# Performance work log

Measured on AMD Instinct MI355X. Metric: run time of the kernel, lower is better.

## Reference

```python
import jax, jax.numpy as jnp
import numpy as np

B, H, S, D = 4, 16, 2048, 64

def setup_inputs() -> dict:
    key = jax.random.key(0)
    kq, kk, kv = jax.random.split(key, 3)
    return {
        "input_query": jax.random.normal(kq, (B, H, S, D), dtype=jnp.float32),
        "input_key": jax.random.normal(kk, (B, H, S, D), dtype=jnp.float32),
        "input_value": jax.random.normal(kv, (B, H, S, D), dtype=jnp.float32),
    }

def reference(input_query, input_key, input_value):
    # Unscaled, unmasked attention: softmax(Q K^T) V
    scores = jnp.einsum("bhsd,bhtd->bhst", input_query, input_key)  # [B,H,S,S]
    probs = jax.nn.softmax(scores, axis=-1)
    return jnp.einsum("bhst,bhtd->bhsd", probs, input_value)  # [B,H,S,D]
```

## Files before the change

kernel.cpp:

```cpp
#include <hip/hip_runtime.h>
#include <hip/hip_bf16.h>
#include <stdint.h>

#define SEQ 2048
#define DIM 64
#define NH  64
#define KT  32
#define NT  (SEQ / KT)
#define RAW_BYTES  16384
#define FRAG_BYTES 12288
#define KF_BYTES   8192

typedef __attribute__((ext_vector_type(8)))  short    bf16x8;
typedef __attribute__((ext_vector_type(8)))  _Float16 f16x8;
typedef __attribute__((ext_vector_type(16))) float    f32x16;
typedef unsigned int u32;

#if __has_builtin(__builtin_amdgcn_exp2f)
#define EXP2(x) __builtin_amdgcn_exp2f(x)
#else
#define EXP2(x) exp2f(x)
#endif

__device__ __forceinline__ int phi(int s) {
    int h = (s >> 2) & 1, b = s >> 3, i = s & 3;
    return 8 * h + 4 * b + i + (b >= 2 ? 8 : 0);
}
__device__ __forceinline__ short f2bf(float f) {
    union { float f; u32 u; } v; v.f = f;
    u32 r = v.u + 0x7fffu + ((v.u >> 16) & 1u);
    return (short)(r >> 16);
}

__device__ __forceinline__ void stage_tile(const float* gK, const float* gV,
                                           char* raw, int wave, int lane) {
    #pragma unroll
    for (int i = 0; i < 2; ++i) {
        const int P  = wave * 128 + i * 64 + lane;
        const int sk = (P & ~15) | ((P & 15) ^ ((P >> 4) & 7));
        char* dK = raw + (size_t)(wave * 128 + i * 64) * 16;
        char* dV = raw + 8192 + (size_t)(wave * 128 + i * 64) * 16;
        __builtin_amdgcn_global_load_lds(
            (const __attribute__((address_space(1))) u32*)((const char*)gK + (size_t)sk * 16),
            (__attribute__((address_space(3))) u32*)dK, 16, 0, 0);
        __builtin_amdgcn_global_load_lds(
            (const __attribute__((address_space(1))) u32*)((const char*)gV + (size_t)P * 16),
            (__attribute__((address_space(3))) u32*)dV, 16, 0, 0);
    }
}

__device__ __forceinline__ void convert_tile(const char* raw, char* frag, int t) {
    const int lane = t & 63, col = lane & 31, h = lane >> 5;
    {
        const int c = t >> 6;
        const int r = phi(col);
        const int kk = 4 * c + 2 * h;
        const float4* rk = (const float4*)raw;
        float4 a = rk[r * 16 + ((kk    ) ^ (r & 7))];
        float4 b = rk[r * 16 + ((kk + 1) ^ (r & 7))];
        float x[8] = {a.x, a.y, a.z, a.w, b.x, b.y, b.z, b.w};
        f16x8 hi, lo;
        #pragma unroll
        for (int j = 0; j < 8; ++j) {
            _Float16 xh = (_Float16)x[j];
            hi[j] = xh;
            lo[j] = (_Float16)(x[j] - (float)xh);
        }
        *(f16x8*)(frag + (c * 2 + 0) * 1024 + lane * 16) = hi;
        *(f16x8*)(frag + (c * 2 + 1) * 1024 + lane * 16) = lo;
    }
    {
        const int f = t >> 7, c = (t >> 6) & 1;
        const float* rv = (const float*)(raw + 8192);
        bf16x8 v;
        #pragma unroll
        for (int j = 0; j < 8; ++j) {
            int key = phi(16 * c + 8 * h + j);
            v[j] = f2bf(rv[key * 64 + f * 32 + col]);
        }
        *(bf16x8*)(frag + KF_BYTES + (f * 2 + c) * 1024 + lane * 16) = v;
    }
}

__global__ __launch_bounds__(256, 2) void attn_fused(
    const float* __restrict__ Q, const float* __restrict__ K,
    const float* __restrict__ V, float* __restrict__ O)
{
    __shared__ __align__(16) char raw[3][RAW_BYTES];
    __shared__ __align__(16) char frag[2][FRAG_BYTES];

    const int tid  = threadIdx.x;
    const int wave = tid >> 6, lane = tid & 63;
    const int h = lane >> 5, col = lane & 31;

    const int bid  = blockIdx.x;
    const int head = (bid & 7) * 8 + ((bid >> 3) & 7);
    const int qb   = (bid >> 6) * 256 + wave * 64;
    const size_t base = (size_t)head * SEQ * DIM;
    const float* Kh = K + base;
    const float* Vh = V + base;

    f16x8 qf[2][4];
    #pragma unroll
    for (int qt = 0; qt < 2; ++qt) {
        const float* qr = Q + base + (size_t)(qb + qt * 32 + col) * DIM;
        #pragma unroll
        for (int c = 0; c < 4; ++c)
            #pragma unroll
            for (int j = 0; j < 8; ++j)
                qf[qt][c][j] = (_Float16)(qr[c * 16 + 8 * h + j] * 1.44269504088896f);
    }

    f32x16 z16;
    #pragma unroll
    for (int r = 0; r < 16; ++r) z16[r] = 0.f;
    f32x16 of[2][2];
    of[0][0] = z16; of[0][1] = z16; of[1][0] = z16; of[1][1] = z16;
    float l_own[2] = {0.f, 0.f};

    stage_tile(Kh, Vh, raw[0], wave, lane);
    stage_tile(Kh + KT * DIM, Vh + KT * DIM, raw[1], wave, lane);
    asm volatile("s_waitcnt vmcnt(4)" ::: "memory");
    __builtin_amdgcn_s_barrier();
    __builtin_amdgcn_sched_barrier(0);
    convert_tile(raw[0], frag[0], tid);

    int stg_i = 2;
    int cvt_i = 1;

    for (int kt = 0; kt < NT; ++kt) {
        asm volatile("s_waitcnt lgkmcnt(0)" ::: "memory");
        __builtin_amdgcn_s_barrier();
        __builtin_amdgcn_sched_barrier(0);

        if (kt + 2 < NT)
            stage_tile(Kh + (size_t)(kt + 2) * KT * DIM,
                       Vh + (size_t)(kt + 2) * KT * DIM, raw[stg_i], wave, lane);
        const char* cur = frag[kt & 1];

        f32x16 s[2]; s[0] = z16; s[1] = z16;
        __builtin_amdgcn_s_setprio(1);
        #pragma unroll
        for (int c = 0; c < 4; ++c) {
            f16x8 kh = *(const f16x8*)(cur + (c * 2 + 0) * 1024 + lane * 16);
            f16x8 kl = *(const f16x8*)(cur + (c * 2 + 1) * 1024 + lane * 16);
            s[0] = __builtin_amdgcn_mfma_f32_32x32x16_f16(kh, qf[0][c], s[0], 0, 0, 0);
            s[0] = __builtin_amdgcn_mfma_f32_32x32x16_f16(kl, qf[0][c], s[0], 0, 0, 0);
            s[1] = __builtin_amdgcn_mfma_f32_32x32x16_f16(kh, qf[1][c], s[1], 0, 0, 0);
            s[1] = __builtin_amdgcn_mfma_f32_32x32x16_f16(kl, qf[1][c], s[1], 0, 0, 0);
        }
        __builtin_amdgcn_s_setprio(0);

        bf16x8 pfrag[2][2];
        #pragma unroll
        for (int qt = 0; qt < 2; ++qt) {
            float p[16], ls = 0.f;
            #pragma unroll
            for (int r = 0; r < 16; ++r) { p[r] = EXP2(s[qt][r]); ls += p[r]; }
            l_own[qt] += ls;
            u32 pk[8], sw[8];
            #pragma unroll
            for (int m = 0; m < 8; ++m) {
                __hip_bfloat162 b2 = __float22bfloat162_rn(make_float2(p[2 * m], p[2 * m + 1]));
                __builtin_memcpy(&pk[m], &b2, 4);
            }
            #pragma unroll
            for (int m = 0; m < 8; ++m) sw[m] = __shfl_xor(pk[m], 32);
            #pragma unroll
            for (int c = 0; c < 2; ++c) {
                union { u32 w[4]; bf16x8 v; } fr;
                fr.w[0] = h ? sw[4 * c + 2] : pk[4 * c + 0];
                fr.w[1] = h ? sw[4 * c + 3] : pk[4 * c + 1];
                fr.w[2] = h ? pk[4 * c + 2] : sw[4 * c + 0];
                fr.w[3] = h ? pk[4 * c + 3] : sw[4 * c + 1];
                pfrag[qt][c] = fr.v;
            }
        }

        __builtin_amdgcn_s_setprio(1);
        #pragma unroll
        for (int f = 0; f < 2; ++f)
            #pragma unroll
            for (int c = 0; c < 2; ++c) {
                bf16x8 vf = *(const bf16x8*)(cur + KF_BYTES + (f * 2 + c) * 1024 + lane * 16);
                of[0][f] = __builtin_amdgcn_mfma_f32_32x32x16_bf16(pfrag[0][c], vf, of[0][f], 0, 0, 0);
                of[1][f] = __builtin_amdgcn_mfma_f32_32x32x16_bf16(pfrag[1][c], vf, of[1][f], 0, 0, 0);
            }
        __builtin_amdgcn_s_setprio(0);

        if (kt + 1 < NT) {
            if (kt + 2 < NT) asm volatile("s_waitcnt vmcnt(4)" ::: "memory");
            else             asm volatile("s_waitcnt vmcnt(0)" ::: "memory");
            __builtin_amdgcn_s_barrier();
            __builtin_amdgcn_sched_barrier(0);
            convert_tile(raw[cvt_i], frag[(kt + 1) & 1], tid);
        }
        stg_i = (stg_i == 2) ? 0 : stg_i + 1;
        cvt_i = (cvt_i == 2) ? 0 : cvt_i + 1;
    }

    float* op = O + base;
    #pragma unroll
    for (int qt = 0; qt < 2; ++qt) {
        float lall = l_own[qt] + __shfl_xor(l_own[qt], 32);
        float inv = 1.0f / lall;
        #pragma unroll
        for (int r = 0; r < 16; ++r) {
            int qrow = (r & 3) + 8 * (r >> 2) + 4 * h;
            float iq = __shfl(inv, qrow);
            op[(size_t)(qb + qt * 32 + qrow) * DIM + col]      = of[qt][0][r] * iq;
            op[(size_t)(qb + qt * 32 + qrow) * DIM + 32 + col] = of[qt][1][r] * iq;
        }
    }
}

extern "C" void kernel_launch(void* const* d_in, const int* in_sizes, int n_in,
                              void* d_out, int out_size, void* d_ws, size_t ws_size,
                              hipStream_t stream) {
    const float* Q = (const float*)d_in[0];
    const float* K = (const float*)d_in[1];
    const float* V = (const float*)d_in[2];
    float* Out = (float*)d_out;
    (void)d_ws; (void)ws_size;

    attn_fused<<<dim3(NH * (SEQ / 256)), dim3(256), 0, stream>>>(Q, K, V, Out);
}
```

Before: 244.5 us.

## Split work across 8 waves per block with 32 query rows per wave

Doubles the block to 512 threads so each wave handles one 32-row query tile instead of two. The K/V staging and fp32-to-fragment conversion are spread over twice as many threads. Each thread then issues one load pair per tile, and convert work is split between the K half and the V half of the block. The aim is lower per-wave register pressure and more waves for latency hiding. The cost is that each K/V fragment read from LDS now feeds only one query tile, which halves reuse and raises the LDS read traffic per MFMA.

```diff
diff --git a/kernel.cpp b/kernel.cpp
--- a/kernel.cpp
+++ b/kernel.cpp
@@ -34,24 +34,21 @@
 
 __device__ __forceinline__ void stage_tile(const float* gK, const float* gV,
                                            char* raw, int wave, int lane) {
-    #pragma unroll
-    for (int i = 0; i < 2; ++i) {
-        const int P  = wave * 128 + i * 64 + lane;
-        const int sk = (P & ~15) | ((P & 15) ^ ((P >> 4) & 7));
-        char* dK = raw + (size_t)(wave * 128 + i * 64) * 16;
-        char* dV = raw + 8192 + (size_t)(wave * 128 + i * 64) * 16;
-        __builtin_amdgcn_global_load_lds(
-            (const __attribute__((address_space(1))) u32*)((const char*)gK + (size_t)sk * 16),
-            (__attribute__((address_space(3))) u32*)dK, 16, 0, 0);
-        __builtin_amdgcn_global_load_lds(
-            (const __attribute__((address_space(1))) u32*)((const char*)gV + (size_t)P * 16),
-            (__attribute__((address_space(3))) u32*)dV, 16, 0, 0);
-    }
+    const int P  = wave * 64 + lane;
+    const int sk = (P & ~15) | ((P & 15) ^ ((P >> 4) & 7));
+    char* dK = raw + (size_t)(wave * 64) * 16;
+    char* dV = raw + 8192 + (size_t)(wave * 64) * 16;
+    __builtin_amdgcn_global_load_lds(
+        (const __attribute__((address_space(1))) u32*)((const char*)gK + (size_t)sk * 16),
+        (__attribute__((address_space(3))) u32*)dK, 16, 0, 0);
+    __builtin_amdgcn_global_load_lds(
+        (const __attribute__((address_space(1))) u32*)((const char*)gV + (size_t)P * 16),
+        (__attribute__((address_space(3))) u32*)dV, 16, 0, 0);
 }
 
 __device__ __forceinline__ void convert_tile(const char* raw, char* frag, int t) {
     const int lane = t & 63, col = lane & 31, h = lane >> 5;
-    {
+    if (t < 256) {
         const int c = t >> 6;
         const int r = phi(col);
         const int kk = 4 * c + 2 * h;
@@ -68,9 +65,9 @@
         }
         *(f16x8*)(frag + (c * 2 + 0) * 1024 + lane * 16) = hi;
         *(f16x8*)(frag + (c * 2 + 1) * 1024 + lane * 16) = lo;
-    }
-    {
-        const int f = t >> 7, c = (t >> 6) & 1;
+    } else {
+        const int u = t - 256;
+        const int f = u >> 7, c = (u >> 6) & 1;
         const float* rv = (const float*)(raw + 8192);
         bf16x8 v;
         #pragma unroll
@@ -82,7 +79,7 @@
     }
 }
 
-__global__ __launch_bounds__(256, 2) void attn_fused(
+__global__ __launch_bounds__(512, 4) void attn_fused(
     const float* __restrict__ Q, const float* __restrict__ K,
     const float* __restrict__ V, float* __restrict__ O)
 {
@@ -95,32 +92,31 @@
 
     const int bid  = blockIdx.x;
     const int head = (bid & 7) * 8 + ((bid >> 3) & 7);
-    const int qb   = (bid >> 6) * 256 + wave * 64;
+    const int qw   = (bid >> 6) * 256 + wave * 32;
     const size_t base = (size_t)head * SEQ * DIM;
     const float* Kh = K + base;
     const float* Vh = V + base;
 
-    f16x8 qf[2][4];
-    #pragma unroll
-    for (int qt = 0; qt < 2; ++qt) {
-        const float* qr = Q + base + (size_t)(qb + qt * 32 + col) * DIM;
+    f16x8 qf[4];
+    {
+        const float* qr = Q + base + (size_t)(qw + col) * DIM;
         #pragma unroll
         for (int c = 0; c < 4; ++c)
             #pragma unroll
             for (int j = 0; j < 8; ++j)
-                qf[qt][c][j] = (_Float16)(qr[c * 16 + 8 * h + j] * 1.44269504088896f);
+                qf[c][j] = (_Float16)(qr[c * 16 + 8 * h + j] * 1.44269504088896f);
     }
 
     f32x16 z16;
     #pragma unroll
     for (int r = 0; r < 16; ++r) z16[r] = 0.f;
-    f32x16 of[2][2];
-    of[0][0] = z16; of[0][1] = z16; of[1][0] = z16; of[1][1] = z16;
-    float l_own[2] = {0.f, 0.f};
+    f32x16 of[2];
+    of[0] = z16; of[1] = z16;
+    float l_own = 0.f;
 
     stage_tile(Kh, Vh, raw[0], wave, lane);
     stage_tile(Kh + KT * DIM, Vh + KT * DIM, raw[1], wave, lane);
-    asm volatile("s_waitcnt vmcnt(4)" ::: "memory");
+    asm volatile("s_waitcnt vmcnt(2)" ::: "memory");
     __builtin_amdgcn_s_barrier();
     __builtin_amdgcn_sched_barrier(0);
     convert_tile(raw[0], frag[0], tid);
@@ -138,26 +134,23 @@
                        Vh + (size_t)(kt + 2) * KT * DIM, raw[stg_i], wave, lane);
         const char* cur = frag[kt & 1];
 
-        f32x16 s[2]; s[0] = z16; s[1] = z16;
+        f32x16 s = z16;
         __builtin_amdgcn_s_setprio(1);
         #pragma unroll
         for (int c = 0; c < 4; ++c) {
             f16x8 kh = *(const f16x8*)(cur + (c * 2 + 0) * 1024 + lane * 16);
             f16x8 kl = *(const f16x8*)(cur + (c * 2 + 1) * 1024 + lane * 16);
-            s[0] = __builtin_amdgcn_mfma_f32_32x32x16_f16(kh, qf[0][c], s[0], 0, 0, 0);
-            s[0] = __builtin_amdgcn_mfma_f32_32x32x16_f16(kl, qf[0][c], s[0], 0, 0, 0);
-            s[1] = __builtin_amdgcn_mfma_f32_32x32x16_f16(kh, qf[1][c], s[1], 0, 0, 0);
-            s[1] = __builtin_amdgcn_mfma_f32_32x32x16_f16(kl, qf[1][c], s[1], 0, 0, 0);
+            s = __builtin_amdgcn_mfma_f32_32x32x16_f16(kh, qf[c], s, 0, 0, 0);
+            s = __builtin_amdgcn_mfma_f32_32x32x16_f16(kl, qf[c], s, 0, 0, 0);
         }
         __builtin_amdgcn_s_setprio(0);
 
-        bf16x8 pfrag[2][2];
-        #pragma unroll
-        for (int qt = 0; qt < 2; ++qt) {
+        bf16x8 pfrag[2];
+        {
             float p[16], ls = 0.f;
             #pragma unroll
-            for (int r = 0; r < 16; ++r) { p[r] = EXP2(s[qt][r]); ls += p[r]; }
-            l_own[qt] += ls;
+            for (int r = 0; r < 16; ++r) { p[r] = EXP2(s[r]); ls += p[r]; }
+            l_own += ls;
             u32 pk[8], sw[8];
             #pragma unroll
             for (int m = 0; m < 8; ++m) {
@@ -173,7 +166,7 @@
                 fr.w[1] = h ? sw[4 * c + 3] : pk[4 * c + 1];
                 fr.w[2] = h ? pk[4 * c + 2] : sw[4 * c + 0];
                 fr.w[3] = h ? pk[4 * c + 3] : sw[4 * c + 1];
-                pfrag[qt][c] = fr.v;
+                pfrag[c] = fr.v;
             }
         }
 
@@ -183,13 +176,12 @@
             #pragma unroll
             for (int c = 0; c < 2; ++c) {
                 bf16x8 vf = *(const bf16x8*)(cur + KF_BYTES + (f * 2 + c) * 1024 + lane * 16);
-                of[0][f] = __builtin_amdgcn_mfma_f32_32x32x16_bf16(pfrag[0][c], vf, of[0][f], 0, 0, 0);
-                of[1][f] = __builtin_amdgcn_mfma_f32_32x32x16_bf16(pfrag[1][c], vf, of[1][f], 0, 0, 0);
+                of[f] = __builtin_amdgcn_mfma_f32_32x32x16_bf16(pfrag[c], vf, of[f], 0, 0, 0);
             }
         __builtin_amdgcn_s_setprio(0);
 
         if (kt + 1 < NT) {
-            if (kt + 2 < NT) asm volatile("s_waitcnt vmcnt(4)" ::: "memory");
+            if (kt + 2 < NT) asm volatile("s_waitcnt vmcnt(2)" ::: "memory");
             else             asm volatile("s_waitcnt vmcnt(0)" ::: "memory");
             __builtin_amdgcn_s_barrier();
             __builtin_amdgcn_sched_barrier(0);
@@ -200,16 +192,15 @@
     }
 
     float* op = O + base;
-    #pragma unroll
-    for (int qt = 0; qt < 2; ++qt) {
-        float lall = l_own[qt] + __shfl_xor(l_own[qt], 32);
+    {
+        float lall = l_own + __shfl_xor(l_own, 32);
         float inv = 1.0f / lall;
         #pragma unroll
         for (int r = 0; r < 16; ++r) {
             int qrow = (r & 3) + 8 * (r >> 2) + 4 * h;
             float iq = __shfl(inv, qrow);
-            op[(size_t)(qb + qt * 32 + qrow) * DIM + col]      = of[qt][0][r] * iq;
-            op[(size_t)(qb + qt * 32 + qrow) * DIM + 32 + col] = of[qt][1][r] * iq;
+            op[(size_t)(qw + qrow) * DIM + col]      = of[0][r] * iq;
+            op[(size_t)(qw + qrow) * DIM + 32 + col] = of[1][r] * iq;
         }
     }
 }
@@ -223,5 +214,5 @@
     float* Out = (float*)d_out;
     (void)d_ws; (void)ws_size;
 
-    attn_fused<<<dim3(NH * (SEQ / 256)), dim3(256), 0, stream>>>(Q, K, V, Out);
-}
+    attn_fused<<<dim3(NH * (SEQ / 256)), dim3(512), 0, stream>>>(Q, K, V, Out);
+}
```

Result: faster. 231.8 us (-5.2%).
